# Performance work log

Hardware: AMD Instinct MI355X
Metric: run time of the kernel (lower is better)

## Reference

```python
import jax, jax.numpy as jnp
import numpy as np

C = 256

def setup_inputs() -> dict:
    key = jax.random.key(0)
    ks = jax.random.split(key, 9)
    B, H, W = 32, 32, 32
    s = C ** -0.5  # init scale for weights
    inputs = jax.random.normal(ks[0], (B, H, W, C), jnp.float32)
    Wq = jax.random.normal(ks[1], (C, C), jnp.float32) * s
    Wk = jax.random.normal(ks[2], (C, C), jnp.float32) * s
    Wv = jax.random.normal(ks[3], (C, C), jnp.float32) * s
    Wo = jax.random.normal(ks[4], (C, C), jnp.float32) * s
    bq = jnp.zeros((C,), jnp.float32)
    bk = jnp.zeros((C,), jnp.float32)
    bv = jnp.zeros((C,), jnp.float32)
    bo = jnp.zeros((C,), jnp.float32)
    return {"inputs": inputs, "Wq": Wq, "bq": bq, "Wk": Wk, "bk": bk,
            "Wv": Wv, "bv": bv, "Wo": Wo, "bo": bo}

def reference(inputs, Wq, bq, Wk, bk, Wv, bv, Wo, bo):
    B, H, W, c = inputs.shape
    scale = jnp.float32(c) ** -0.5
    x = inputs.reshape(B, H * W, c)           # 1x1 conv == per-pixel matmul
    q = x @ Wq + bq                           # [B, HW, C]
    k = x @ Wk + bk
    v = x @ Wv + bv
    scores = jnp.einsum('bnc,bmc->bnm', q, k) * scale  # [B, HW, HW]
    attn = jax.nn.softmax(scores, axis=-1)
    attended = jnp.einsum('bnm,bmc->bnc', attn, v)     # [B, HW, C]
    out = attended @ Wo + bo
    return out.reshape(B, H, W, c)
```

## Files before the change

### kernel.cpp

```cpp
#include <hip/hip_runtime.h>
#include <hip/hip_bf16.h>

typedef __bf16 bf16;
typedef __bf16 bf16x8 __attribute__((ext_vector_type(8)));
typedef float f32x4 __attribute__((ext_vector_type(4)));

#define SM_C 0.09016994374947424f

__global__ __launch_bounds__(256) void transpose_w(
    const float* __restrict__ Wq, const float* __restrict__ Wk,
    const float* __restrict__ Wv, const float* __restrict__ Wo,
    bf16* __restrict__ Wt)
{
    int idx = blockIdx.x * 256 + threadIdx.x;
    int m = idx >> 16, r = idx & 65535;
    int n = r >> 8, k = r & 255;
    const float* W = (m == 0) ? Wq : (m == 1) ? Wk : (m == 2) ? Wv : Wo;
    Wt[(size_t)m * 65536 + n * 256 + k] = (bf16)W[k * 256 + n];
}

__global__ __launch_bounds__(512, 2) void qkv_gemm(
    const float* __restrict__ X, const bf16* __restrict__ Wt,
    const float* __restrict__ bq, const float* __restrict__ bk,
    const float* __restrict__ bv,
    bf16* __restrict__ Qo, bf16* __restrict__ Ko, bf16* __restrict__ Vto)
{
    __shared__ bf16 Xs[128 * 264];
    __shared__ bf16 Ws[2][64 * 264];

    const int t    = threadIdx.x;
    const int lane = t & 63, wv = t >> 6;
    const int quad = lane >> 4, l16 = lane & 15;
    const int bm   = blockIdx.x;

#pragma unroll
    for (int i = 0; i < 8; ++i) {
        int c = t + i * 512;
        int row = c >> 5, cf = (c & 31) * 8;
        const float* px = X + (size_t)(bm * 128 + row) * 256 + cf;
        f32x4 a = *(const f32x4*)px, b = *(const f32x4*)(px + 4);
        bf16x8 r;
#pragma unroll
        for (int j = 0; j < 4; ++j) { r[j] = (bf16)a[j]; r[j + 4] = (bf16)b[j]; }
        *(bf16x8*)(Xs + row * 264 + cf) = r;
    }

    bf16x8 wreg[4];
#pragma unroll
    for (int i = 0; i < 4; ++i) {
        int c = t + i * 512;
        wreg[i] = *(const bf16x8*)(Wt + (size_t)(c >> 5) * 256 + (c & 31) * 8);
    }
#pragma unroll
    for (int i = 0; i < 4; ++i) {
        int c = t + i * 512;
        *(bf16x8*)(Ws[0] + (c >> 5) * 264 + (c & 31) * 8) = wreg[i];
    }
#pragma unroll
    for (int i = 0; i < 4; ++i) {
        int c = t + i * 512;
        wreg[i] = *(const bf16x8*)(Wt + (size_t)16384 + (c >> 5) * 256 + (c & 31) * 8);
    }

    for (int o = 0; o < 12; ++o) {
        __syncthreads();

        if (o < 11) {
#pragma unroll
            for (int i = 0; i < 4; ++i) {
                int c = t + i * 512;
                *(bf16x8*)(Ws[(o + 1) & 1] + (c >> 5) * 264 + (c & 31) * 8) = wreg[i];
            }
            if (o < 10) {
#pragma unroll
                for (int i = 0; i < 4; ++i) {
                    int c = t + i * 512;
                    wreg[i] = *(const bf16x8*)(Wt + (size_t)(o + 2) * 16384 + (c >> 5) * 256 + (c & 31) * 8);
                }
            }
        }

        const bf16* Wb = Ws[o & 1];
        const f32x4 zero = {0.0f, 0.0f, 0.0f, 0.0f};
        f32x4 acc[4];
        acc[0] = zero; acc[1] = zero; acc[2] = zero; acc[3] = zero;

#pragma unroll
        for (int ks = 0; ks < 8; ++ks) {
            bf16x8 a = *(const bf16x8*)(Xs + (wv * 16 + l16) * 264 + ks * 32 + quad * 8);
#pragma unroll
            for (int nt = 0; nt < 4; ++nt) {
                bf16x8 bb = *(const bf16x8*)(Wb + (nt * 16 + l16) * 264 + ks * 32 + quad * 8);
                acc[nt] = __builtin_amdgcn_mfma_f32_16x16x32_bf16(a, bb, acc[nt], 0, 0, 0);
            }
        }

        const int proj = o >> 2, nt4 = o & 3;
        const float* bias = (proj == 0) ? bq : (proj == 1) ? bk : bv;
#pragma unroll
        for (int nt = 0; nt < 4; ++nt) {
            int col = nt4 * 64 + nt * 16 + l16;
            float bvv = bias[col];
#pragma unroll
            for (int r = 0; r < 4; ++r) {
                int grow = bm * 128 + wv * 16 + quad * 4 + r;
                float v = acc[nt][r] + bvv;
                if (proj == 0) {
                    Qo[(size_t)grow * 256 + col] = (bf16)v;
                } else if (proj == 1) {
                    Ko[(size_t)grow * 256 + col] = (bf16)v;
                } else {
                    int b = grow >> 10, m = grow & 1023;
                    Vto[(size_t)b * 262144 + (size_t)col * 1024 + m] = (bf16)v;
                }
            }
        }
    }
}

__global__ __launch_bounds__(512, 2) void flash_attn(
    const bf16* __restrict__ Qr, const bf16* __restrict__ K,
    const bf16* __restrict__ Vt, bf16* __restrict__ A)
{
    __shared__ bf16 Ks[2][32 * 264];
    __shared__ bf16 Vs[2][256 * 40];
    __shared__ bf16 Ps[8][16 * 32];

    const int t    = threadIdx.x;
    const int lane = t & 63, wv = t >> 6;
    const int quad = lane >> 4, l16 = lane & 15;
    const int b  = blockIdx.x;
    const int qt = blockIdx.y;

    bf16x8 qf[8];
    const size_t qrow = (size_t)b * 1024 + qt * 128 + wv * 16 + l16;
#pragma unroll
    for (int ks = 0; ks < 8; ++ks)
        qf[ks] = *(const bf16x8*)(Qr + qrow * 256 + ks * 32 + quad * 8);

    const f32x4 zero = {0.0f, 0.0f, 0.0f, 0.0f};
    f32x4 o[16];
#pragma unroll
    for (int n = 0; n < 16; ++n) o[n] = zero;
    float lst[4] = {0.f, 0.f, 0.f, 0.f};

    char* Pb = (char*)(Ps[wv]);

    const int kv0 = t >> 4, kc0 = (t & 15) * 8;
    const int vc0 = t >> 1, vm0 = (t & 1) * 8;

    bf16x8 kp[2], vp[2];
#pragma unroll
    for (int p = 0; p < 2; ++p) {
        kp[p] = *(const bf16x8*)(K + (size_t)(b * 1024 + kv0) * 256 + kc0 + p * 128);
        vp[p] = *(const bf16x8*)(Vt + (size_t)b * 262144 + (size_t)vc0 * 1024 + vm0 + p * 16);
    }
#pragma unroll
    for (int p = 0; p < 2; ++p) {
        *(bf16x8*)(Ks[0] + kv0 * 264 + kc0 + p * 128) = kp[p];
        *(bf16x8*)(Vs[0] + vc0 * 40 + vm0 + p * 16) = vp[p];
    }
#pragma unroll
    for (int p = 0; p < 2; ++p) {
        kp[p] = *(const bf16x8*)(K + (size_t)(b * 1024 + 32 + kv0) * 256 + kc0 + p * 128);
        vp[p] = *(const bf16x8*)(Vt + (size_t)b * 262144 + (size_t)vc0 * 1024 + 32 + vm0 + p * 16);
    }

    for (int j = 0; j < 32; ++j) {
        const bf16* Kb = Ks[j & 1];
        const bf16* Vb = Vs[j & 1];
        __syncthreads();

        f32x4 s[2];
        s[0] = zero; s[1] = zero;
#pragma unroll
        for (int ks = 0; ks < 8; ++ks) {
#pragma unroll
            for (int n = 0; n < 2; ++n) {
                bf16x8 bfr = *(const bf16x8*)(Kb + (n * 16 + l16) * 264 + ks * 32 + quad * 8);
                s[n] = __builtin_amdgcn_mfma_f32_16x16x32_bf16(qf[ks], bfr, s[n], 0, 0, 0);
            }
        }

        if (j < 31) {
            bf16* Kn = Ks[(j + 1) & 1];
            bf16* Vn = Vs[(j + 1) & 1];
#pragma unroll
            for (int p = 0; p < 2; ++p) {
                *(bf16x8*)(Kn + kv0 * 264 + kc0 + p * 128) = kp[p];
                *(bf16x8*)(Vn + vc0 * 40 + vm0 + p * 16) = vp[p];
            }
            if (j < 30) {
#pragma unroll
                for (int p = 0; p < 2; ++p) {
                    kp[p] = *(const bf16x8*)(K + (size_t)(b * 1024 + (j + 2) * 32 + kv0) * 256 + kc0 + p * 128);
                    vp[p] = *(const bf16x8*)(Vt + (size_t)b * 262144 + (size_t)vc0 * 1024 + (j + 2) * 32 + vm0 + p * 16);
                }
            }
        }

#pragma unroll
        for (int n = 0; n < 2; ++n) {
#pragma unroll
            for (int r = 0; r < 4; ++r) {
                float pv = __builtin_amdgcn_exp2f(s[n][r] * SM_C);
                lst[r] += pv;
                int row = quad * 4 + r;
                *(bf16*)(Pb + ((row * 64 + n * 32 + l16 * 2) ^ ((row & 7) << 4))) = (bf16)pv;
            }
        }

        bf16x8 af = *(const bf16x8*)(Pb + ((l16 * 64 + quad * 16) ^ ((l16 & 7) << 4)));
#pragma unroll
        for (int n = 0; n < 16; ++n) {
            bf16x8 bfr = *(const bf16x8*)(Vb + (n * 16 + l16) * 40 + quad * 8);
            o[n] = __builtin_amdgcn_mfma_f32_16x16x32_bf16(af, bfr, o[n], 0, 0, 0);
        }
    }

#pragma unroll
    for (int r = 0; r < 4; ++r) {
        float l = lst[r];
        for (int off = 1; off < 16; off <<= 1)
            l += __shfl_xor(l, off, 64);
        float inv = 1.0f / l;
        size_t grow = (size_t)b * 1024 + qt * 128 + wv * 16 + quad * 4 + r;
#pragma unroll
        for (int n = 0; n < 16; ++n)
            A[grow * 256 + n * 16 + l16] = (bf16)(o[n][r] * inv);
    }
}

__global__ __launch_bounds__(256) void oproj_gemm(
    const bf16* __restrict__ Xv, const bf16* __restrict__ W,
    const float* __restrict__ bias, float* __restrict__ outv)
{
    __shared__ bf16 Xs[128 * 72];
    __shared__ bf16 Ws[64 * 72];

    const int t    = threadIdx.x;
    const int lane = t & 63, wv = t >> 6;
    const int quad = lane >> 4, l16 = lane & 15;
    const int bm = blockIdx.x;
    const int bn = blockIdx.y;

    const f32x4 zero = {0.0f, 0.0f, 0.0f, 0.0f};
    f32x4 acc[2][4];
    for (int i = 0; i < 2; ++i)
        for (int j = 0; j < 4; ++j) acc[i][j] = zero;

    const int m0 = t >> 3;
    const int c0 = (t & 7) * 8;

    bf16x8 xp[4], wp[2];
#pragma unroll
    for (int p = 0; p < 4; ++p)
        xp[p] = *(const bf16x8*)(Xv + (size_t)(bm * 128 + m0 + p * 32) * 256 + c0);
#pragma unroll
    for (int p = 0; p < 2; ++p)
        wp[p] = *(const bf16x8*)(W + (size_t)(bn * 64 + m0 + p * 32) * 256 + c0);

    for (int kt = 0; kt < 4; ++kt) {
#pragma unroll
        for (int p = 0; p < 4; ++p)
            *(bf16x8*)(Xs + (m0 + p * 32) * 72 + c0) = xp[p];
#pragma unroll
        for (int p = 0; p < 2; ++p)
            *(bf16x8*)(Ws + (m0 + p * 32) * 72 + c0) = wp[p];
        __syncthreads();

        if (kt < 3) {
#pragma unroll
            for (int p = 0; p < 4; ++p)
                xp[p] = *(const bf16x8*)(Xv + (size_t)(bm * 128 + m0 + p * 32) * 256 + (kt + 1) * 64 + c0);
#pragma unroll
            for (int p = 0; p < 2; ++p)
                wp[p] = *(const bf16x8*)(W + (size_t)(bn * 64 + m0 + p * 32) * 256 + (kt + 1) * 64 + c0);
        }

#pragma unroll
        for (int ks = 0; ks < 2; ++ks) {
            bf16x8 a[2], bb[4];
            for (int mt = 0; mt < 2; ++mt)
                a[mt] = *(const bf16x8*)(Xs + (wv * 32 + mt * 16 + l16) * 72 + ks * 32 + quad * 8);
            for (int nt = 0; nt < 4; ++nt)
                bb[nt] = *(const bf16x8*)(Ws + (nt * 16 + l16) * 72 + ks * 32 + quad * 8);
            for (int mt = 0; mt < 2; ++mt)
                for (int nt = 0; nt < 4; ++nt)
                    acc[mt][nt] = __builtin_amdgcn_mfma_f32_16x16x32_bf16(
                        a[mt], bb[nt], acc[mt][nt], 0, 0, 0);
        }
        __syncthreads();
    }

#pragma unroll
    for (int nt = 0; nt < 4; ++nt) {
        int col = bn * 64 + nt * 16 + l16;
        float bvv = bias[col];
#pragma unroll
        for (int mt = 0; mt < 2; ++mt)
#pragma unroll
            for (int r = 0; r < 4; ++r) {
                int grow = bm * 128 + wv * 32 + mt * 16 + quad * 4 + r;
                outv[(size_t)grow * 256 + col] = acc[mt][nt][r] + bvv;
            }
    }
}

extern "C" void kernel_launch(void* const* d_in, const int* in_sizes, int n_in,
                              void* d_out, int out_size, void* d_ws, size_t ws_size,
                              hipStream_t stream)
{
    (void)in_sizes; (void)n_in; (void)out_size; (void)ws_size;
    const float* X  = (const float*)d_in[0];
    const float* Wq = (const float*)d_in[1];
    const float* bq = (const float*)d_in[2];
    const float* Wk = (const float*)d_in[3];
    const float* bk = (const float*)d_in[4];
    const float* Wv = (const float*)d_in[5];
    const float* bv = (const float*)d_in[6];
    const float* Wo = (const float*)d_in[7];
    const float* bo = (const float*)d_in[8];
    float* out = (float*)d_out;

    const size_t NTOK = (size_t)32768 * 256;

    bf16* Wt  = (bf16*)d_ws;
    bf16* Qw  = (bf16*)d_ws + 262144;
    bf16* Kw  = Qw + NTOK;
    bf16* Vtw = Kw + NTOK;

    transpose_w<<<1024, 256, 0, stream>>>(Wq, Wk, Wv, Wo, Wt);
    qkv_gemm   <<<256,  512, 0, stream>>>(X, Wt, bq, bk, bv, Qw, Kw, Vtw);
    flash_attn <<<dim3(32, 8),  512, 0, stream>>>(Qw, Kw, Vtw, Qw);
    oproj_gemm <<<dim3(256, 4), 256, 0, stream>>>(Qw, Wt + 3 * 65536, bo, out);
}
```

Measured before the change: 187.0 us.

## Retile QKV GEMM over a 2D grid with K-chunked staging, add MFMA priority hints

The QKV projection kernel drops the single block per row tile that looped over all 12 output column chunks. It now uses a 2D grid of 256x6 blocks, each computing a 128x128 output tile. Each block streams K in 64-wide chunks with register prefetch, gives each warp 2x8 MFMA tiles, and writes V transposed with packed 4-element stores. This aims to add parallelism and occupancy and to raise MFMA reuse per LDS load, at the cost of converting X to bf16 six times, once per column block. The flash attention kernel also wraps its MFMA loops in s_setprio to favour matrix work over other waves' memory traffic.

```diff
diff --git a/kernel.cpp b/kernel.cpp
--- a/kernel.cpp
+++ b/kernel.cpp
@@ -2,6 +2,7 @@
 #include <hip/hip_bf16.h>
 
 typedef __bf16 bf16;
+typedef __bf16 bf16x4 __attribute__((ext_vector_type(4)));
 typedef __bf16 bf16x8 __attribute__((ext_vector_type(8)));
 typedef float f32x4 __attribute__((ext_vector_type(4)));
 
@@ -19,100 +20,100 @@
     Wt[(size_t)m * 65536 + n * 256 + k] = (bf16)W[k * 256 + n];
 }
 
-__global__ __launch_bounds__(512, 2) void qkv_gemm(
+__global__ __launch_bounds__(256, 3) void qkv_gemm(
     const float* __restrict__ X, const bf16* __restrict__ Wt,
     const float* __restrict__ bq, const float* __restrict__ bk,
     const float* __restrict__ bv,
     bf16* __restrict__ Qo, bf16* __restrict__ Ko, bf16* __restrict__ Vto)
 {
-    __shared__ bf16 Xs[128 * 264];
-    __shared__ bf16 Ws[2][64 * 264];
+    __shared__ bf16 Xs[128 * 72];
+    __shared__ bf16 Ws_[128 * 72];
 
     const int t    = threadIdx.x;
     const int lane = t & 63, wv = t >> 6;
     const int quad = lane >> 4, l16 = lane & 15;
     const int bm   = blockIdx.x;
-
-#pragma unroll
-    for (int i = 0; i < 8; ++i) {
-        int c = t + i * 512;
-        int row = c >> 5, cf = (c & 31) * 8;
-        const float* px = X + (size_t)(bm * 128 + row) * 256 + cf;
-        f32x4 a = *(const f32x4*)px, b = *(const f32x4*)(px + 4);
-        bf16x8 r;
-#pragma unroll
-        for (int j = 0; j < 4; ++j) { r[j] = (bf16)a[j]; r[j + 4] = (bf16)b[j]; }
-        *(bf16x8*)(Xs + row * 264 + cf) = r;
-    }
-
-    bf16x8 wreg[4];
-#pragma unroll
-    for (int i = 0; i < 4; ++i) {
-        int c = t + i * 512;
-        wreg[i] = *(const bf16x8*)(Wt + (size_t)(c >> 5) * 256 + (c & 31) * 8);
-    }
-#pragma unroll
-    for (int i = 0; i < 4; ++i) {
-        int c = t + i * 512;
-        *(bf16x8*)(Ws[0] + (c >> 5) * 264 + (c & 31) * 8) = wreg[i];
-    }
-#pragma unroll
-    for (int i = 0; i < 4; ++i) {
-        int c = t + i * 512;
-        wreg[i] = *(const bf16x8*)(Wt + (size_t)16384 + (c >> 5) * 256 + (c & 31) * 8);
-    }
-
-    for (int o = 0; o < 12; ++o) {
-        __syncthreads();
-
-        if (o < 11) {
-#pragma unroll
-            for (int i = 0; i < 4; ++i) {
-                int c = t + i * 512;
-                *(bf16x8*)(Ws[(o + 1) & 1] + (c >> 5) * 264 + (c & 31) * 8) = wreg[i];
-            }
-            if (o < 10) {
-#pragma unroll
-                for (int i = 0; i < 4; ++i) {
-                    int c = t + i * 512;
-                    wreg[i] = *(const bf16x8*)(Wt + (size_t)(o + 2) * 16384 + (c >> 5) * 256 + (c & 31) * 8);
-                }
-            }
-        }
-
-        const bf16* Wb = Ws[o & 1];
-        const f32x4 zero = {0.0f, 0.0f, 0.0f, 0.0f};
-        f32x4 acc[4];
-        acc[0] = zero; acc[1] = zero; acc[2] = zero; acc[3] = zero;
-
-#pragma unroll
-        for (int ks = 0; ks < 8; ++ks) {
-            bf16x8 a = *(const bf16x8*)(Xs + (wv * 16 + l16) * 264 + ks * 32 + quad * 8);
-#pragma unroll
-            for (int nt = 0; nt < 4; ++nt) {
-                bf16x8 bb = *(const bf16x8*)(Wb + (nt * 16 + l16) * 264 + ks * 32 + quad * 8);
-                acc[nt] = __builtin_amdgcn_mfma_f32_16x16x32_bf16(a, bb, acc[nt], 0, 0, 0);
-            }
-        }
-
-        const int proj = o >> 2, nt4 = o & 3;
-        const float* bias = (proj == 0) ? bq : (proj == 1) ? bk : bv;
-#pragma unroll
-        for (int nt = 0; nt < 4; ++nt) {
-            int col = nt4 * 64 + nt * 16 + l16;
-            float bvv = bias[col];
-#pragma unroll
-            for (int r = 0; r < 4; ++r) {
-                int grow = bm * 128 + wv * 16 + quad * 4 + r;
-                float v = acc[nt][r] + bvv;
-                if (proj == 0) {
-                    Qo[(size_t)grow * 256 + col] = (bf16)v;
-                } else if (proj == 1) {
-                    Ko[(size_t)grow * 256 + col] = (bf16)v;
-                } else {
-                    int b = grow >> 10, m = grow & 1023;
-                    Vto[(size_t)b * 262144 + (size_t)col * 1024 + m] = (bf16)v;
-                }
+    const int bn   = blockIdx.y;
+    const int proj = bn >> 1;
+
+    const bf16* W = Wt + (size_t)proj * 65536 + (size_t)(bn & 1) * 32768;
+    const float* bias = (proj == 0) ? bq : (proj == 1) ? bk : bv;
+
+    const int m0 = t >> 3;
+    const int c0 = (t & 7) * 8;
+
+    const f32x4 zero = {0.0f, 0.0f, 0.0f, 0.0f};
+    f32x4 acc[2][8];
+#pragma unroll
+    for (int i = 0; i < 2; ++i)
+#pragma unroll
+        for (int j = 0; j < 8; ++j) acc[i][j] = zero;
+
+    f32x4 xa[4], xb[4]; bf16x8 wp[4];
+#pragma unroll
+    for (int p = 0; p < 4; ++p) {
+        const float* px = X + (size_t)(bm * 128 + m0 + p * 32) * 256 + c0;
+        xa[p] = *(const f32x4*)px; xb[p] = *(const f32x4*)(px + 4);
+        wp[p] = *(const bf16x8*)(W + (size_t)(m0 + p * 32) * 256 + c0);
+    }
+
+    for (int kt = 0; kt < 4; ++kt) {
+#pragma unroll
+        for (int p = 0; p < 4; ++p) {
+            bf16x8 r;
+#pragma unroll
+            for (int j = 0; j < 4; ++j) { r[j] = (bf16)xa[p][j]; r[j + 4] = (bf16)xb[p][j]; }
+            *(bf16x8*)(Xs + (m0 + p * 32) * 72 + c0) = r;
+            *(bf16x8*)(Ws_ + (m0 + p * 32) * 72 + c0) = wp[p];
+        }
+        __syncthreads();
+
+        if (kt < 3) {
+#pragma unroll
+            for (int p = 0; p < 4; ++p) {
+                const float* px = X + (size_t)(bm * 128 + m0 + p * 32) * 256 + (kt + 1) * 64 + c0;
+                xa[p] = *(const f32x4*)px; xb[p] = *(const f32x4*)(px + 4);
+                wp[p] = *(const bf16x8*)(W + (size_t)(m0 + p * 32) * 256 + (kt + 1) * 64 + c0);
+            }
+        }
+
+#pragma unroll
+        for (int ks = 0; ks < 2; ++ks) {
+            bf16x8 a[2], bb[8];
+#pragma unroll
+            for (int mt = 0; mt < 2; ++mt)
+                a[mt] = *(const bf16x8*)(Xs + (wv * 32 + mt * 16 + l16) * 72 + ks * 32 + quad * 8);
+#pragma unroll
+            for (int nt = 0; nt < 8; ++nt)
+                bb[nt] = *(const bf16x8*)(Ws_ + (nt * 16 + l16) * 72 + ks * 32 + quad * 8);
+#pragma unroll
+            for (int mt = 0; mt < 2; ++mt)
+#pragma unroll
+                for (int nt = 0; nt < 8; ++nt)
+                    acc[mt][nt] = __builtin_amdgcn_mfma_f32_16x16x32_bf16(
+                        a[mt], bb[nt], acc[mt][nt], 0, 0, 0);
+        }
+        __syncthreads();
+    }
+
+#pragma unroll
+    for (int nt = 0; nt < 8; ++nt) {
+        int col = (bn & 1) * 128 + nt * 16 + l16;
+        float bvv = bias[col];
+#pragma unroll
+        for (int mt = 0; mt < 2; ++mt) {
+            int grow0 = bm * 128 + wv * 32 + mt * 16 + quad * 4;
+            if (proj == 2) {
+                bf16x4 pk;
+#pragma unroll
+                for (int r = 0; r < 4; ++r) pk[r] = (bf16)(acc[mt][nt][r] + bvv);
+                int b = grow0 >> 10, m = grow0 & 1023;
+                *(bf16x4*)(Vto + (size_t)b * 262144 + (size_t)col * 1024 + m) = pk;
+            } else {
+                bf16* dst = (proj == 0) ? Qo : Ko;
+#pragma unroll
+                for (int r = 0; r < 4; ++r)
+                    dst[(size_t)(grow0 + r) * 256 + col] = (bf16)(acc[mt][nt][r] + bvv);
             }
         }
     }
@@ -173,6 +174,7 @@
 
         f32x4 s[2];
         s[0] = zero; s[1] = zero;
+        __builtin_amdgcn_s_setprio(1);
 #pragma unroll
         for (int ks = 0; ks < 8; ++ks) {
 #pragma unroll
@@ -181,6 +183,7 @@
                 s[n] = __builtin_amdgcn_mfma_f32_16x16x32_bf16(qf[ks], bfr, s[n], 0, 0, 0);
             }
         }
+        __builtin_amdgcn_s_setprio(0);
 
         if (j < 31) {
             bf16* Kn = Ks[(j + 1) & 1];
@@ -211,11 +214,13 @@
         }
 
         bf16x8 af = *(const bf16x8*)(Pb + ((l16 * 64 + quad * 16) ^ ((l16 & 7) << 4)));
+        __builtin_amdgcn_s_setprio(1);
 #pragma unroll
         for (int n = 0; n < 16; ++n) {
             bf16x8 bfr = *(const bf16x8*)(Vb + (n * 16 + l16) * 40 + quad * 8);
             o[n] = __builtin_amdgcn_mfma_f32_16x16x32_bf16(af, bfr, o[n], 0, 0, 0);
         }
+        __builtin_amdgcn_s_setprio(0);
     }
 
 #pragma unroll
@@ -331,7 +336,7 @@
     bf16* Vtw = Kw + NTOK;
 
     transpose_w<<<1024, 256, 0, stream>>>(Wq, Wk, Wv, Wo, Wt);
-    qkv_gemm   <<<256,  512, 0, stream>>>(X, Wt, bq, bk, bv, Qw, Kw, Vtw);
+    qkv_gemm   <<<dim3(256, 6), 256, 0, stream>>>(X, Wt, bq, bk, bv, Qw, Kw, Vtw);
     flash_attn <<<dim3(32, 8),  512, 0, stream>>>(Qw, Kw, Vtw, Qw);
     oproj_gemm <<<dim3(256, 4), 256, 0, stream>>>(Qw, Wt + 3 * 65536, bo, out);
 }
```

Result: no change. 187.7 us (+0.4%).
